# Kernel tuning notes

Hardware: AMD Instinct MI355X
Metric: run time of the kernel (lower is better)

## Reference

```python
import jax, jax.numpy as jnp
import numpy as np

B, N, D = 2, 2048, 1024
RANK, HEADS = 256, 16
HS = RANK // HEADS          # 16, low-rank head size for QK
DH = D // HEADS             # 64, value head size
SCALE = 1.0 / np.sqrt(HS)


def setup_inputs() -> dict:
    key = jax.random.key(0)
    k1, k2, k3 = jax.random.split(key, 3)
    x = jax.random.normal(k1, (B, N, D), dtype=jnp.float32)
    # causal additive mask, 0 on/below diag, -1e9 above
    mask = jnp.where(jnp.tril(jnp.ones((N, N), dtype=bool)), 0.0, -1e9).astype(jnp.float32)
    Wqk = jax.random.normal(k2, (2 * RANK, D), dtype=jnp.float32) * (1.0 / np.sqrt(D))
    Wv = jax.random.normal(k3, (D, D), dtype=jnp.float32) * (1.0 / np.sqrt(D))
    return {"x": x, "mask": mask, "Wqk": Wqk, "Wv": Wv}


def reference(x, mask, Wqk, Wv):
    b, n, d = x.shape
    qk = jnp.einsum('bnd,rd->bnr', x, Wqk)            # [b,n,2*rank]
    q, k = jnp.split(qk, 2, axis=-1)                  # [b,n,rank] each
    # L2 normalize over FULL rank dim (before head split), clamp norm >= 1e-6
    q = q / jnp.maximum(jnp.linalg.norm(q, axis=-1, keepdims=True), 1e-6)
    k = k / jnp.maximum(jnp.linalg.norm(k, axis=-1, keepdims=True), 1e-6)
    q = q.reshape(b, n, HEADS, HS).transpose(0, 2, 1, 3)   # [b,h,n,hs]
    k = k.reshape(b, n, HEADS, HS).transpose(0, 2, 1, 3)
    v = jnp.einsum('bnd,ed->bne', x, Wv).reshape(b, n, HEADS, DH).transpose(0, 2, 1, 3)  # [b,h,n,dh]
    att = jnp.einsum('bhqe,bhke->bhqk', q, k) * SCALE
    att = jnp.clip(att, -10000.0, 10000.0)
    att = att + mask[None, None, :, :]
    att = jax.nn.softmax(att, axis=-1)
    # NaN guard: zero NaNs then renormalize (no-op when no NaNs)
    att = jnp.where(jnp.isnan(att), 0.0, att)
    att = att / jnp.maximum(att.sum(axis=-1, keepdims=True), 1e-6)
    y = jnp.einsum('bhqk,bhkd->bhqd', att, v)              # [b,h,n,dh]
    return y.transpose(0, 2, 1, 3).reshape(b, n, d)
```

## Files before the change

kernel.cpp:

```cpp
#include <hip/hip_runtime.h>
#include <math.h>

#define BATCH 2
#define SEQ   2048
#define DIM   1024
#define RANK  256
#define HEADS 16
#define HS    16
#define DH    64
#define MROWS 4096

#define QSCALE 0.36067376f

typedef __attribute__((ext_vector_type(8)))  short    short8;
typedef __attribute__((ext_vector_type(4)))  float    f32x4;
typedef __attribute__((ext_vector_type(16))) float    f32x16;
typedef __attribute__((ext_vector_type(2)))  unsigned uint2v;

#define GPTR const __attribute__((address_space(1))) unsigned int*
#define LPTR __attribute__((address_space(3))) unsigned int*

__device__ __forceinline__ unsigned short f2bf(float f) {
    union { float f; unsigned u; } v; v.f = f;
    return (unsigned short)((v.u + 0x7FFFu + ((v.u >> 16) & 1u)) >> 16);
}
__device__ __forceinline__ float bf2f(unsigned short h) {
    union { unsigned u; float f; } v; v.u = ((unsigned)h) << 16;
    return v.f;
}

#define XQ   1048576
#define WQKQ 131072
#define WVQ  262144
__global__ __launch_bounds__(256) void conv3(const float* __restrict__ x,
                                             const float* __restrict__ wqk,
                                             const float* __restrict__ wv,
                                             unsigned short* __restrict__ xb,
                                             unsigned short* __restrict__ wcat)
{
    const int i = blockIdx.x * 256 + threadIdx.x;
    const float* src; unsigned short* dst; int j;
    if (i < XQ)              { src = x;   dst = xb;   j = i; }
    else if (i < XQ + WQKQ)  { src = wqk; dst = wcat; j = i - XQ; }
    else                     { src = wv;  dst = wcat + (size_t)4 * WQKQ; j = i - XQ - WQKQ; }
    float4 v = ((const float4*)src)[j];
    ushort4 o; o.x = f2bf(v.x); o.y = f2bf(v.y); o.z = f2bf(v.z); o.w = f2bf(v.w);
    ((ushort4*)dst)[j] = o;
}

__global__ __launch_bounds__(256, 3) void gemm_mfma(const unsigned short* __restrict__ A,
                                                    const unsigned short* __restrict__ W,
                                                    unsigned short* __restrict__ qkb,
                                                    unsigned short* __restrict__ vt)
{
    __shared__ __align__(16) unsigned short Alds[2][128 * 64];
    __shared__ __align__(16) unsigned short Blds[2][64 * 64];

    const int tid = threadIdx.x;
    const int w = tid >> 6, lane = tid & 63;
    const int lr = lane & 15, lg = lane >> 4;
    const int wm = w >> 1, wn = w & 1;

    const int Lf = blockIdx.x;
    const int wg = (Lf & 7) * 96 + (Lf >> 3);
    const int bm = (wg & 31) * 128;
    const int bn = (wg >> 5) * 64;

    const int rs = lane >> 3, cs = lane & 7;

    f32x4 acc[4][2] = {};

#define STAGEG(kt_, buf_) do {                                                        \
        const int k0_ = (kt_) * 64;                                                   \
        _Pragma("unroll")                                                             \
        for (int i = 0; i < 4; ++i) {                                                 \
            const int r = w * 32 + i * 8 + rs;                                        \
            __builtin_amdgcn_global_load_lds(                                         \
                (GPTR)&A[(size_t)(bm + r) * 1024 + k0_ + 8 * (cs ^ (r & 7))],         \
                (LPTR)&Alds[buf_][(w * 32 + i * 8) * 64], 16, 0, 0);                  \
        }                                                                             \
        _Pragma("unroll")                                                             \
        for (int i = 0; i < 2; ++i) {                                                 \
            const int r = w * 16 + i * 8 + rs;                                        \
            __builtin_amdgcn_global_load_lds(                                         \
                (GPTR)&W[(size_t)(bn + r) * 1024 + k0_ + 8 * (cs ^ (r & 7))],         \
                (LPTR)&Blds[buf_][(w * 16 + i * 8) * 64], 16, 0, 0);                  \
        }                                                                             \
    } while (0)

    STAGEG(0, 0);

    #pragma unroll 1
    for (int kt = 0; kt < 16; ++kt) {
        if (kt + 1 < 16) {
            STAGEG(kt + 1, (kt + 1) & 1);
            asm volatile("s_waitcnt vmcnt(6)" ::: "memory");
        } else {
            asm volatile("s_waitcnt vmcnt(0)" ::: "memory");
        }
        __builtin_amdgcn_sched_barrier(0);
        __builtin_amdgcn_s_barrier();

        const int buf = kt & 1;
        #pragma unroll
        for (int kk = 0; kk < 2; ++kk) {
            short8 af[4], bfr[2];
            #pragma unroll
            for (int mi = 0; mi < 4; ++mi) {
                const int row = wm * 64 + mi * 16 + lr;
                af[mi] = *(const short8*)&Alds[buf][row * 64 + 8 * ((kk * 4 + lg) ^ (row & 7))];
            }
            #pragma unroll
            for (int ni = 0; ni < 2; ++ni) {
                const int row = wn * 32 + ni * 16 + lr;
                bfr[ni] = *(const short8*)&Blds[buf][row * 64 + 8 * ((kk * 4 + lg) ^ (row & 7))];
            }
            #pragma unroll
            for (int mi = 0; mi < 4; ++mi)
                #pragma unroll
                for (int ni = 0; ni < 2; ++ni)
                    acc[mi][ni] = __builtin_amdgcn_mfma_f32_16x16x32_bf16(af[mi], bfr[ni], acc[mi][ni], 0, 0, 0);
        }
        __builtin_amdgcn_s_barrier();
    }
#undef STAGEG

    if (bn < 512) {
        #pragma unroll
        for (int mi = 0; mi < 4; ++mi) {
            const int rbase = bm + wm * 64 + mi * 16 + lg * 4;
            #pragma unroll
            for (int ni = 0; ni < 2; ++ni) {
                const int col = bn + wn * 32 + ni * 16 + lr;
                #pragma unroll
                for (int r = 0; r < 4; ++r)
                    qkb[(size_t)(rbase + r) * 512 + col] = f2bf(acc[mi][ni][r]);
            }
        }
    } else {
        const int nb = bn - 512;
        #pragma unroll
        for (int mi = 0; mi < 4; ++mi) {
            const int m = bm + wm * 64 + mi * 16 + lg * 4;
            const int bb = m >> 11, ms = m & 2047;
            #pragma unroll
            for (int ni = 0; ni < 2; ++ni) {
                const int d = nb + wn * 32 + ni * 16 + lr;
                ushort4 pk;
                pk.x = f2bf(acc[mi][ni][0]); pk.y = f2bf(acc[mi][ni][1]);
                pk.z = f2bf(acc[mi][ni][2]); pk.w = f2bf(acc[mi][ni][3]);
                *(ushort4*)&vt[((size_t)bb * DIM + d) * SEQ + ms] = pk;
            }
        }
    }
}

__global__ __launch_bounds__(256) void l2norm_split(const unsigned short* __restrict__ qkb,
                                                    unsigned short* __restrict__ qn,
                                                    unsigned short* __restrict__ kn)
{
    const int row = blockIdx.x;
    const int t = threadIdx.x;
    const unsigned short* p = qkb + (size_t)row * 512;
    float q = bf2f(p[t]);
    float k = bf2f(p[t + 256]);
    float sq = q * q, sk = k * k;
    #pragma unroll
    for (int off = 32; off > 0; off >>= 1) {
        sq += __shfl_down(sq, off);
        sk += __shfl_down(sk, off);
    }
    __shared__ float sh[8];
    const int wid = t >> 6;
    if ((t & 63) == 0) { sh[wid * 2] = sq; sh[wid * 2 + 1] = sk; }
    __syncthreads();
    sq = sh[0] + sh[2] + sh[4] + sh[6];
    sk = sh[1] + sh[3] + sh[5] + sh[7];
    const float rq = QSCALE / fmaxf(sqrtf(sq), 1e-6f);
    const float rk = 1.0f   / fmaxf(sqrtf(sk), 1e-6f);

    const int b = row >> 11, n = row & 2047;
    const int head = t >> 4, hs = t & 15;
    const size_t o = (((size_t)b * HEADS + head) * SEQ + n) * 16 + hs;
    qn[o] = f2bf(q * rq);
    kn[o] = f2bf(k * rk);
}


template<bool MASK>
__device__ __forceinline__ void segpv(const short8 ak0, const short8 ak1, const short8 bq,
                                      const unsigned short* Vs, int kb, int kh, int hi,
                                      int l31, int qg, f32x16 o[2], float& lp)
{
    const f32x16 z = {};
    short8 pa[4];

    const f32x16 s0 = __builtin_amdgcn_mfma_f32_32x32x16_bf16(ak0, bq, z, 0, 0, 0);
    {
        float p0[16];
        #pragma unroll
        for (int r = 0; r < 16; ++r) {
            float e = __builtin_exp2f(s0[r]);
            if (MASK) {
                const int kl = kb + (r & 3) + 8 * (r >> 2) + 4 * hi;
                e = (kl > qg) ? 0.0f : e;
            }
            p0[r] = e; lp += e;
        }
        #pragma unroll
        for (int g = 0; g < 2; ++g) {
            const int jj = 2 * g;
            unsigned a0, a1, b0, b1;
            asm("v_cvt_pk_bf16_f32 %0, %1, %2" : "=v"(a0) : "v"(p0[4*jj]),     "v"(p0[4*jj + 1]));
            asm("v_cvt_pk_bf16_f32 %0, %1, %2" : "=v"(b0) : "v"(p0[4*jj + 2]), "v"(p0[4*jj + 3]));
            asm("v_cvt_pk_bf16_f32 %0, %1, %2" : "=v"(a1) : "v"(p0[4*jj + 4]), "v"(p0[4*jj + 5]));
            asm("v_cvt_pk_bf16_f32 %0, %1, %2" : "=v"(b1) : "v"(p0[4*jj + 6]), "v"(p0[4*jj + 7]));
            const uint2v r0 = __builtin_amdgcn_permlane32_swap(a0, a1, false, false);
            const uint2v r1 = __builtin_amdgcn_permlane32_swap(b0, b1, false, false);
            union { short8 s; unsigned u[4]; } pu;
            pu.u[0] = r0[0]; pu.u[1] = r1[0]; pu.u[2] = r0[1]; pu.u[3] = r1[1];
            pa[g] = pu.s;
        }
    }
    const f32x16 s1 = __builtin_amdgcn_mfma_f32_32x32x16_bf16(ak1, bq, z, 0, 0, 0);
    {
        float p1[16];
        #pragma unroll
        for (int r = 0; r < 16; ++r) {
            float e = __builtin_exp2f(s1[r]);
            if (MASK) {
                const int kl = kb + 32 + (r & 3) + 8 * (r >> 2) + 4 * hi;
                e = (kl > qg) ? 0.0f : e;
            }
            p1[r] = e; lp += e;
        }
        #pragma unroll
        for (int g = 0; g < 2; ++g) {
            const int jj = 2 * g;
            unsigned a0, a1, b0, b1;
            asm("v_cvt_pk_bf16_f32 %0, %1, %2" : "=v"(a0) : "v"(p1[4*jj]),     "v"(p1[4*jj + 1]));
            asm("v_cvt_pk_bf16_f32 %0, %1, %2" : "=v"(b0) : "v"(p1[4*jj + 2]), "v"(p1[4*jj + 3]));
            asm("v_cvt_pk_bf16_f32 %0, %1, %2" : "=v"(a1) : "v"(p1[4*jj + 4]), "v"(p1[4*jj + 5]));
            asm("v_cvt_pk_bf16_f32 %0, %1, %2" : "=v"(b1) : "v"(p1[4*jj + 6]), "v"(p1[4*jj + 7]));
            const uint2v r0 = __builtin_amdgcn_permlane32_swap(a0, a1, false, false);
            const uint2v r1 = __builtin_amdgcn_permlane32_swap(b0, b1, false, false);
            union { short8 s; unsigned u[4]; } pu;
            pu.u[0] = r0[0]; pu.u[1] = r1[0]; pu.u[2] = r0[1]; pu.u[3] = r1[1];
            pa[2 + g] = pu.s;
        }
    }

    #pragma unroll
    for (int g = 0; g < 4; ++g)
        #pragma unroll
        for (int half = 0; half < 2; ++half) {
            const int row = half * 32 + l31;
            const int slot = (8 * kh + 2 * g + hi) ^ (row & 15);
            const short8 bv = *(const short8*)&Vs[row * 128 + 8 * slot];
            o[half] = __builtin_amdgcn_mfma_f32_32x32x16_bf16(pa[g], bv, o[half], 0, 0, 0);
        }
}

__global__ __launch_bounds__(512, 4) void attn_w8(const unsigned short* __restrict__ qn,
                                                  const unsigned short* __restrict__ kn,
                                                  const unsigned short* __restrict__ vt,
                                                  float* __restrict__ out)
{
    const int L = blockIdx.x;
    const int bh = L & 31;
    const int p  = L >> 5;
    const int h = bh & 15, b = bh >> 4;

    const int tid = threadIdx.x, w = tid >> 6, lane = tid & 63;
    const int seg = w >> 2, qh = (w >> 1) & 1, kh = w & 1;
    const int l31 = lane & 31, hi = lane >> 5;

    const int qt  = seg ? p : 31 - p;
    const int nts = (qt >> 1) + 1;
    const int nt0 = ((31 - p) >> 1) + 1;
    const int band = qt * 64 + qh * 32;
    const int qg = band + l31;

    __shared__ __align__(16) unsigned char smem[33792];

    const unsigned short* qbh = qn + (size_t)bh * SEQ * 16;
    const unsigned short* kbh = kn + (size_t)bh * SEQ * 16;

    const short8 bq = *(const short8*)&qbh[qg * 16 + 8 * hi];

    f32x16 o[2] = {};
    float lp = 0.0f;

    const unsigned short* kwin = kbh + (64 * kh + l31) * 16 + 8 * hi;
    short8 ak0 = *(const short8*)(kwin);
    short8 ak1 = *(const short8*)(kwin + 32 * 16);

    const int vsub = lane >> 4, vslot = lane & 15;

#define STAGEV(kt_, buf_) do {                                                                    \
        const int k0_ = (kt_) * 128;                                                              \
        _Pragma("unroll")                                                                         \
        for (int i = 0; i < 2; ++i) {                                                             \
            const int c = 2 * w + i;                                                              \
            const int dh = 4 * c + vsub;                                                          \
            const int so = 8 * (vslot ^ (dh & 15));                                               \
            __builtin_amdgcn_global_load_lds(                                                     \
                (GPTR)&vt[((size_t)b * DIM + h * DH + dh) * SEQ + k0_ + so],                      \
                (LPTR)(smem + (buf_) * 16384 + c * 1024), 16, 0, 0);                              \
        }                                                                                         \
    } while (0)

    STAGEV(0, 0);

    #pragma unroll 1
    for (int kt = 0; kt < nt0; ++kt) {
        short8 an0 = ak0, an1 = ak1;
        if (kt + 1 < nt0) {
            STAGEV(kt + 1, (kt + 1) & 1);
            an0 = *(const short8*)(kwin + (size_t)(kt + 1) * 128 * 16);
            an1 = *(const short8*)(kwin + (size_t)(kt + 1) * 128 * 16 + 32 * 16);
            asm volatile("s_waitcnt vmcnt(4)" ::: "memory");
        } else {
            asm volatile("s_waitcnt vmcnt(0)" ::: "memory");
        }
        __builtin_amdgcn_sched_barrier(0);
        __builtin_amdgcn_s_barrier();

        if (kt < nts) {
            const unsigned short* Vs = (const unsigned short*)(smem + (kt & 1) * 16384);
            const int kb = kt * 128 + 64 * kh;
            __builtin_amdgcn_s_setprio(1);
            if (kt < nts - 1) {
                segpv<false>(ak0, ak1, bq, Vs, kb, kh, hi, l31, qg, o, lp);
            } else if (kb <= band + 31) {
                if (kb + 63 <= band) segpv<false>(ak0, ak1, bq, Vs, kb, kh, hi, l31, qg, o, lp);
                else                 segpv<true >(ak0, ak1, bq, Vs, kb, kh, hi, l31, qg, o, lp);
            }
            __builtin_amdgcn_s_setprio(0);
        }

        ak0 = an0; ak1 = an1;
        __builtin_amdgcn_s_barrier();
    }
#undef STAGEV

    lp += __shfl_xor(lp, 32);

    __syncthreads();
    float* Os = (float*)(smem + seg * 16384);
    float* Ls = (float*)(smem + 32768 + seg * 512);

    if (kh == 1) {
        #pragma unroll
        for (int half = 0; half < 2; ++half)
            #pragma unroll
            for (int r = 0; r < 16; ++r) {
                const int q = (r & 3) + 8 * (r >> 2) + 4 * hi;
                Os[(qh * 32 + q) * 64 + half * 32 + l31] = o[half][r];
            }
        Ls[qh * 64 + lane] = lp;
    }
    __syncthreads();
    if (kh == 0) {
        const float lt = lp + Ls[qh * 64 + lane];
        const float inv = 1.0f / fmaxf(lt, 1e-6f);
        #pragma unroll
        for (int r = 0; r < 16; ++r) {
            const int q = (r & 3) + 8 * (r >> 2) + 4 * hi;
            const float iv = __shfl(inv, q);
            #pragma unroll
            for (int half = 0; half < 2; ++half) {
                const float v = (o[half][r] + Os[(qh * 32 + q) * 64 + half * 32 + l31]) * iv;
                __builtin_nontemporal_store(v,
                    &out[((size_t)b * SEQ + band + q) * DIM + h * DH + half * 32 + l31]);
            }
        }
    }
}

extern "C" void kernel_launch(void* const* d_in, const int* in_sizes, int n_in,
                              void* d_out, int out_size, void* d_ws, size_t ws_size,
                              hipStream_t stream)
{
    const float* x   = (const float*)d_in[0];
    const float* Wqk = (const float*)d_in[2];
    const float* Wv  = (const float*)d_in[3];
    float* out = (float*)d_out;

    unsigned short* xb   = (unsigned short*)d_ws;
    unsigned short* qkb  = xb  + (size_t)MROWS * DIM;
    unsigned short* vt   = qkb + (size_t)MROWS * 512;
    unsigned short* wcat = vt  + (size_t)BATCH * DIM * SEQ;
    unsigned short* qn = xb;
    unsigned short* kn = xb + (size_t)32 * SEQ * 16;

    conv3<<<5632, 256, 0, stream>>>(x, Wqk, Wv, xb, wcat);
    gemm_mfma<<<768, 256, 0, stream>>>(xb, wcat, qkb, vt);
    l2norm_split<<<MROWS, 256, 0, stream>>>(qkb, qn, kn);
    attn_w8<<<512, 512, 0, stream>>>(qn, kn, vt, out);
}
```

Before: 68.74 us.

## Pre-swizzle V into MFMA fragment layout and drop LDS staging in attention

The GEMM epilogue now writes V in a per-head tiled layout that matches the MFMA B-operand fragments, so the attention kernel can load V directly from global memory into registers. The attention kernel is restructured so each wave owns a whole 32-query band over all key tiles, with band assignments balanced across the causal triangle, and runs 256 threads per block. This removes the LDS double buffering, the barriers and the cross-wave reduction of partial outputs. In exchange every wave reads V from global/L2 itself with no sharing, and there is no explicit prefetch overlap for the V loads.

```diff
diff --git a/kernel.cpp b/kernel.cpp
--- a/kernel.cpp
+++ b/kernel.cpp
@@ -51,7 +51,7 @@
 __global__ __launch_bounds__(256, 3) void gemm_mfma(const unsigned short* __restrict__ A,
                                                     const unsigned short* __restrict__ W,
                                                     unsigned short* __restrict__ qkb,
-                                                    unsigned short* __restrict__ vt)
+                                                    unsigned short* __restrict__ vt2)
 {
     __shared__ __align__(16) unsigned short Alds[2][128 * 64];
     __shared__ __align__(16) unsigned short Blds[2][64 * 64];
@@ -142,14 +142,19 @@
         #pragma unroll
         for (int mi = 0; mi < 4; ++mi) {
             const int m = bm + wm * 64 + mi * 16 + lg * 4;
-            const int bb = m >> 11, ms = m & 2047;
+            const int bb = m >> 11, k = m & 2047;
             #pragma unroll
             for (int ni = 0; ni < 2; ++ni) {
                 const int d = nb + wn * 32 + ni * 16 + lr;
+                const int h = d >> 6, dh = d & 63;
                 ushort4 pk;
                 pk.x = f2bf(acc[mi][ni][0]); pk.y = f2bf(acc[mi][ni][1]);
                 pk.z = f2bf(acc[mi][ni][2]); pk.w = f2bf(acc[mi][ni][3]);
-                *(ushort4*)&vt[((size_t)bb * DIM + d) * SEQ + ms] = pk;
+                const size_t off = (size_t)(bb * HEADS + h) * (SEQ * 64)
+                                 + (k >> 6) * 4096 + ((k >> 4) & 3) * 1024
+                                 + (dh >> 5) * 512 + (dh & 31) * 16
+                                 + ((k >> 3) & 1) * 8 + (k & 7);
+                *(ushort4*)&vt2[off] = pk;
             }
         }
     }
@@ -188,9 +193,8 @@
 
 
 template<bool MASK>
-__device__ __forceinline__ void segpv(const short8 ak0, const short8 ak1, const short8 bq,
-                                      const unsigned short* Vs, int kb, int kh, int hi,
-                                      int l31, int qg, f32x16 o[2], float& lp)
+__device__ __forceinline__ void tile_nb(const short8 ak0, const short8 ak1, const short8 bq,
+                                        const short8 vb[4][2], int hi, f32x16 o[2], float& lp)
 {
     const f32x16 z = {};
     short8 pa[4];
@@ -202,11 +206,13 @@
         for (int r = 0; r < 16; ++r) {
             float e = __builtin_exp2f(s0[r]);
             if (MASK) {
-                const int kl = kb + (r & 3) + 8 * (r >> 2) + 4 * hi;
-                e = (kl > qg) ? 0.0f : e;
-            }
-            p0[r] = e; lp += e;
-        }
+                const int kl = (r & 3) + 8 * (r >> 2) + 4 * hi;
+                e = (kl > 0) ? 0.0f : e;
+            }
+            p0[r] = e;
+        }
+        #pragma unroll
+        for (int r = 0; r < 16; ++r) lp += p0[r];
         #pragma unroll
         for (int g = 0; g < 2; ++g) {
             const int jj = 2 * g;
@@ -227,11 +233,7 @@
         float p1[16];
         #pragma unroll
         for (int r = 0; r < 16; ++r) {
-            float e = __builtin_exp2f(s1[r]);
-            if (MASK) {
-                const int kl = kb + 32 + (r & 3) + 8 * (r >> 2) + 4 * hi;
-                e = (kl > qg) ? 0.0f : e;
-            }
+            const float e = __builtin_exp2f(s1[r]);
             p1[r] = e; lp += e;
         }
         #pragma unroll
@@ -253,127 +255,118 @@
     #pragma unroll
     for (int g = 0; g < 4; ++g)
         #pragma unroll
-        for (int half = 0; half < 2; ++half) {
-            const int row = half * 32 + l31;
-            const int slot = (8 * kh + 2 * g + hi) ^ (row & 15);
-            const short8 bv = *(const short8*)&Vs[row * 128 + 8 * slot];
-            o[half] = __builtin_amdgcn_mfma_f32_32x32x16_bf16(pa[g], bv, o[half], 0, 0, 0);
-        }
-}
-
-__global__ __launch_bounds__(512, 4) void attn_w8(const unsigned short* __restrict__ qn,
+        for (int half = 0; half < 2; ++half)
+            o[half] = __builtin_amdgcn_mfma_f32_32x32x16_bf16(pa[g], vb[g][half], o[half], 0, 0, 0);
+}
+
+__device__ __forceinline__ void tile_nb_mask(const short8 ak0, const short8 ak1, const short8 bq,
+                                             const short8 vb[4][2], int kb, int hi, int qg,
+                                             f32x16 o[2], float& lp)
+{
+    const f32x16 z = {};
+    short8 pa[4];
+    const f32x16 s0 = __builtin_amdgcn_mfma_f32_32x32x16_bf16(ak0, bq, z, 0, 0, 0);
+    const f32x16 s1 = __builtin_amdgcn_mfma_f32_32x32x16_bf16(ak1, bq, z, 0, 0, 0);
+    float p0[16], p1[16];
+    #pragma unroll
+    for (int r = 0; r < 16; ++r) {
+        const int kl = kb + (r & 3) + 8 * (r >> 2) + 4 * hi;
+        float e0 = __builtin_exp2f(s0[r]);
+        float e1 = __builtin_exp2f(s1[r]);
+        e0 = (kl > qg) ? 0.0f : e0;
+        e1 = (kl + 32 > qg) ? 0.0f : e1;
+        p0[r] = e0; p1[r] = e1;
+        lp += e0 + e1;
+    }
+    #pragma unroll
+    for (int g = 0; g < 4; ++g) {
+        const float* pc = (g < 2) ? p0 : p1;
+        const int jj = 2 * (g & 1);
+        unsigned a0, a1, b0, b1;
+        asm("v_cvt_pk_bf16_f32 %0, %1, %2" : "=v"(a0) : "v"(pc[4*jj]),     "v"(pc[4*jj + 1]));
+        asm("v_cvt_pk_bf16_f32 %0, %1, %2" : "=v"(b0) : "v"(pc[4*jj + 2]), "v"(pc[4*jj + 3]));
+        asm("v_cvt_pk_bf16_f32 %0, %1, %2" : "=v"(a1) : "v"(pc[4*jj + 4]), "v"(pc[4*jj + 5]));
+        asm("v_cvt_pk_bf16_f32 %0, %1, %2" : "=v"(b1) : "v"(pc[4*jj + 6]), "v"(pc[4*jj + 7]));
+        const uint2v r0 = __builtin_amdgcn_permlane32_swap(a0, a1, false, false);
+        const uint2v r1 = __builtin_amdgcn_permlane32_swap(b0, b1, false, false);
+        union { short8 s; unsigned u[4]; } pu;
+        pu.u[0] = r0[0]; pu.u[1] = r1[0]; pu.u[2] = r0[1]; pu.u[3] = r1[1];
+        pa[g] = pu.s;
+    }
+    #pragma unroll
+    for (int g = 0; g < 4; ++g)
+        #pragma unroll
+        for (int half = 0; half < 2; ++half)
+            o[half] = __builtin_amdgcn_mfma_f32_32x32x16_bf16(pa[g], vb[g][half], o[half], 0, 0, 0);
+}
+
+__global__ __launch_bounds__(256, 2) void attn_nb(const unsigned short* __restrict__ qn,
                                                   const unsigned short* __restrict__ kn,
-                                                  const unsigned short* __restrict__ vt,
+                                                  const unsigned short* __restrict__ vt2,
                                                   float* __restrict__ out)
 {
     const int L = blockIdx.x;
     const int bh = L & 31;
-    const int p  = L >> 5;
+    const int j  = L >> 5;
     const int h = bh & 15, b = bh >> 4;
 
     const int tid = threadIdx.x, w = tid >> 6, lane = tid & 63;
-    const int seg = w >> 2, qh = (w >> 1) & 1, kh = w & 1;
     const int l31 = lane & 31, hi = lane >> 5;
 
-    const int qt  = seg ? p : 31 - p;
-    const int nts = (qt >> 1) + 1;
-    const int nt0 = ((31 - p) >> 1) + 1;
-    const int band = qt * 64 + qh * 32;
-    const int qg = band + l31;
-
-    __shared__ __align__(16) unsigned char smem[33792];
+    const int band = (w == 0) ? j : (w == 1) ? 63 - j : (w == 2) ? 31 - j : 32 + j;
+    const int nts = (band >> 1) + 1;
+    const int qg = band * 32 + l31;
 
     const unsigned short* qbh = qn + (size_t)bh * SEQ * 16;
     const unsigned short* kbh = kn + (size_t)bh * SEQ * 16;
-
-    const short8 bq = *(const short8*)&qbh[qg * 16 + 8 * hi];
+    const unsigned short* vbh = vt2 + (size_t)bh * (SEQ * 64);
+
+    const short8 bq = *(const short8*)&qbh[(size_t)qg * 16 + 8 * hi];
 
     f32x16 o[2] = {};
     float lp = 0.0f;
 
-    const unsigned short* kwin = kbh + (64 * kh + l31) * 16 + 8 * hi;
+    const unsigned short* kwin = kbh + l31 * 16 + 8 * hi;
+    const unsigned short* vwin = vbh + l31 * 16 + hi * 8;
+
     short8 ak0 = *(const short8*)(kwin);
     short8 ak1 = *(const short8*)(kwin + 32 * 16);
 
-    const int vsub = lane >> 4, vslot = lane & 15;
-
-#define STAGEV(kt_, buf_) do {                                                                    \
-        const int k0_ = (kt_) * 128;                                                              \
-        _Pragma("unroll")                                                                         \
-        for (int i = 0; i < 2; ++i) {                                                             \
-            const int c = 2 * w + i;                                                              \
-            const int dh = 4 * c + vsub;                                                          \
-            const int so = 8 * (vslot ^ (dh & 15));                                               \
-            __builtin_amdgcn_global_load_lds(                                                     \
-                (GPTR)&vt[((size_t)b * DIM + h * DH + dh) * SEQ + k0_ + so],                      \
-                (LPTR)(smem + (buf_) * 16384 + c * 1024), 16, 0, 0);                              \
-        }                                                                                         \
-    } while (0)
-
-    STAGEV(0, 0);
-
     #pragma unroll 1
-    for (int kt = 0; kt < nt0; ++kt) {
+    for (int t = 0; t < nts; ++t) {
+        short8 vb[4][2];
+        #pragma unroll
+        for (int g = 0; g < 4; ++g)
+            #pragma unroll
+            for (int half = 0; half < 2; ++half)
+                vb[g][half] = *(const short8*)(vwin + (size_t)t * 4096 + g * 1024 + half * 512);
+
         short8 an0 = ak0, an1 = ak1;
-        if (kt + 1 < nt0) {
-            STAGEV(kt + 1, (kt + 1) & 1);
-            an0 = *(const short8*)(kwin + (size_t)(kt + 1) * 128 * 16);
-            an1 = *(const short8*)(kwin + (size_t)(kt + 1) * 128 * 16 + 32 * 16);
-            asm volatile("s_waitcnt vmcnt(4)" ::: "memory");
-        } else {
-            asm volatile("s_waitcnt vmcnt(0)" ::: "memory");
-        }
-        __builtin_amdgcn_sched_barrier(0);
-        __builtin_amdgcn_s_barrier();
-
-        if (kt < nts) {
-            const unsigned short* Vs = (const unsigned short*)(smem + (kt & 1) * 16384);
-            const int kb = kt * 128 + 64 * kh;
-            __builtin_amdgcn_s_setprio(1);
-            if (kt < nts - 1) {
-                segpv<false>(ak0, ak1, bq, Vs, kb, kh, hi, l31, qg, o, lp);
-            } else if (kb <= band + 31) {
-                if (kb + 63 <= band) segpv<false>(ak0, ak1, bq, Vs, kb, kh, hi, l31, qg, o, lp);
-                else                 segpv<true >(ak0, ak1, bq, Vs, kb, kh, hi, l31, qg, o, lp);
-            }
-            __builtin_amdgcn_s_setprio(0);
-        }
+        if (t + 1 < nts) {
+            an0 = *(const short8*)(kwin + (size_t)(t + 1) * 1024);
+            an1 = *(const short8*)(kwin + (size_t)(t + 1) * 1024 + 32 * 16);
+        }
+
+        if (t < nts - 1)
+            tile_nb<false>(ak0, ak1, bq, vb, hi, o, lp);
+        else
+            tile_nb_mask(ak0, ak1, bq, vb, t * 64, hi, qg, o, lp);
 
         ak0 = an0; ak1 = an1;
-        __builtin_amdgcn_s_barrier();
-    }
-#undef STAGEV
+    }
 
     lp += __shfl_xor(lp, 32);
-
-    __syncthreads();
-    float* Os = (float*)(smem + seg * 16384);
-    float* Ls = (float*)(smem + 32768 + seg * 512);
-
-    if (kh == 1) {
-        #pragma unroll
-        for (int half = 0; half < 2; ++half)
-            #pragma unroll
-            for (int r = 0; r < 16; ++r) {
-                const int q = (r & 3) + 8 * (r >> 2) + 4 * hi;
-                Os[(qh * 32 + q) * 64 + half * 32 + l31] = o[half][r];
-            }
-        Ls[qh * 64 + lane] = lp;
-    }
-    __syncthreads();
-    if (kh == 0) {
-        const float lt = lp + Ls[qh * 64 + lane];
-        const float inv = 1.0f / fmaxf(lt, 1e-6f);
-        #pragma unroll
-        for (int r = 0; r < 16; ++r) {
-            const int q = (r & 3) + 8 * (r >> 2) + 4 * hi;
-            const float iv = __shfl(inv, q);
-            #pragma unroll
-            for (int half = 0; half < 2; ++half) {
-                const float v = (o[half][r] + Os[(qh * 32 + q) * 64 + half * 32 + l31]) * iv;
-                __builtin_nontemporal_store(v,
-                    &out[((size_t)b * SEQ + band + q) * DIM + h * DH + half * 32 + l31]);
-            }
+    const float inv = 1.0f / fmaxf(lp, 1e-6f);
+
+    #pragma unroll
+    for (int r = 0; r < 16; ++r) {
+        const int q = (r & 3) + 8 * (r >> 2) + 4 * hi;
+        const float iv = __shfl(inv, q);
+        #pragma unroll
+        for (int half = 0; half < 2; ++half) {
+            const float v = o[half][r] * iv;
+            __builtin_nontemporal_store(v,
+                &out[((size_t)b * SEQ + band * 32 + q) * DIM + h * DH + half * 32 + l31]);
         }
     }
 }
@@ -389,13 +382,13 @@
 
     unsigned short* xb   = (unsigned short*)d_ws;
     unsigned short* qkb  = xb  + (size_t)MROWS * DIM;
-    unsigned short* vt   = qkb + (size_t)MROWS * 512;
-    unsigned short* wcat = vt  + (size_t)BATCH * DIM * SEQ;
+    unsigned short* vt2  = qkb + (size_t)MROWS * 512;
+    unsigned short* wcat = vt2 + (size_t)BATCH * DIM * SEQ;
     unsigned short* qn = xb;
     unsigned short* kn = xb + (size_t)32 * SEQ * 16;
 
     conv3<<<5632, 256, 0, stream>>>(x, Wqk, Wv, xb, wcat);
-    gemm_mfma<<<768, 256, 0, stream>>>(xb, wcat, qkb, vt);
+    gemm_mfma<<<768, 256, 0, stream>>>(xb, wcat, qkb, vt2);
     l2norm_split<<<MROWS, 256, 0, stream>>>(qkb, qn, kn);
-    attn_w8<<<512, 512, 0, stream>>>(qn, kn, vt, out);
-}
+    attn_nb<<<512, 256, 0, stream>>>(qn, kn, vt2, out);
+}
```

Result: slower. 72.79 us (+5.9%).

## Fuse fp32-to-bf16 conversion into GEMM staging, drop separate convert kernel

Applied to the files above, without the earlier changes.

Removes the conv3 kernel and has the GEMM load fp32 x and weights directly into registers, convert them with packed bf16 conversion instructions, and write them into swizzled LDS. This saves one launch and the bf16 round trip through global memory. In exchange, the GEMM now reads twice as many bytes per tile and each of the 768 blocks re-converts its tiles. The async global-to-LDS path is also replaced by register-staged prefetch, which adds register pressure and uses a single barrier per iteration.

```diff
diff --git a/kernel.cpp b/kernel.cpp
--- a/kernel.cpp
+++ b/kernel.cpp
@@ -29,29 +29,11 @@
     return v.f;
 }
 
-#define XQ   1048576
-#define WQKQ 131072
-#define WVQ  262144
-__global__ __launch_bounds__(256) void conv3(const float* __restrict__ x,
-                                             const float* __restrict__ wqk,
-                                             const float* __restrict__ wv,
-                                             unsigned short* __restrict__ xb,
-                                             unsigned short* __restrict__ wcat)
-{
-    const int i = blockIdx.x * 256 + threadIdx.x;
-    const float* src; unsigned short* dst; int j;
-    if (i < XQ)              { src = x;   dst = xb;   j = i; }
-    else if (i < XQ + WQKQ)  { src = wqk; dst = wcat; j = i - XQ; }
-    else                     { src = wv;  dst = wcat + (size_t)4 * WQKQ; j = i - XQ - WQKQ; }
-    float4 v = ((const float4*)src)[j];
-    ushort4 o; o.x = f2bf(v.x); o.y = f2bf(v.y); o.z = f2bf(v.z); o.w = f2bf(v.w);
-    ((ushort4*)dst)[j] = o;
-}
-
-__global__ __launch_bounds__(256, 3) void gemm_mfma(const unsigned short* __restrict__ A,
-                                                    const unsigned short* __restrict__ W,
-                                                    unsigned short* __restrict__ qkb,
-                                                    unsigned short* __restrict__ vt)
+__global__ __launch_bounds__(256, 3) void gemm_fused(const float* __restrict__ A,
+                                                     const float* __restrict__ Wqk,
+                                                     const float* __restrict__ Wv,
+                                                     unsigned short* __restrict__ qkb,
+                                                     unsigned short* __restrict__ vt)
 {
     __shared__ __align__(16) unsigned short Alds[2][128 * 64];
     __shared__ __align__(16) unsigned short Blds[2][64 * 64];
@@ -66,39 +48,49 @@
     const int bm = (wg & 31) * 128;
     const int bn = (wg >> 5) * 64;
 
-    const int rs = lane >> 3, cs = lane & 7;
+    const float* Wsrc = (bn < 512) ? (Wqk + (size_t)bn * 1024)
+                                   : (Wv + (size_t)(bn - 512) * 1024);
+
+    const int rsub = tid >> 4;
+    const int kq   = tid & 15;
+
+    float4 avreg[8], bvreg[4];
+
+#define LOADF(kt_) do { const int k0_ = (kt_) * 64;                                               \
+        _Pragma("unroll") for (int jj = 0; jj < 8; ++jj)                                          \
+            avreg[jj] = *(const float4*)&A[(size_t)(bm + jj * 16 + rsub) * 1024 + k0_ + 4 * kq];  \
+        _Pragma("unroll") for (int jj = 0; jj < 4; ++jj)                                          \
+            bvreg[jj] = *(const float4*)&Wsrc[(size_t)(jj * 16 + rsub) * 1024 + k0_ + 4 * kq];    \
+    } while (0)
+
+#define CVTWR(buf_) do {                                                                          \
+        _Pragma("unroll") for (int jj = 0; jj < 8; ++jj) {                                        \
+            const int r = jj * 16 + rsub;                                                         \
+            unsigned u0, u1;                                                                      \
+            asm("v_cvt_pk_bf16_f32 %0, %1, %2" : "=v"(u0) : "v"(avreg[jj].x), "v"(avreg[jj].y));  \
+            asm("v_cvt_pk_bf16_f32 %0, %1, %2" : "=v"(u1) : "v"(avreg[jj].z), "v"(avreg[jj].w));  \
+            uint2 pkv; pkv.x = u0; pkv.y = u1;                                                    \
+            *(uint2*)((char*)&Alds[buf_][0] + r * 128 + 16 * ((kq >> 1) ^ (r & 7)) + 8 * (kq & 1)) = pkv; \
+        }                                                                                         \
+        _Pragma("unroll") for (int jj = 0; jj < 4; ++jj) {                                        \
+            const int r = jj * 16 + rsub;                                                         \
+            unsigned u0, u1;                                                                      \
+            asm("v_cvt_pk_bf16_f32 %0, %1, %2" : "=v"(u0) : "v"(bvreg[jj].x), "v"(bvreg[jj].y));  \
+            asm("v_cvt_pk_bf16_f32 %0, %1, %2" : "=v"(u1) : "v"(bvreg[jj].z), "v"(bvreg[jj].w));  \
+            uint2 pkv; pkv.x = u0; pkv.y = u1;                                                    \
+            *(uint2*)((char*)&Blds[buf_][0] + r * 128 + 16 * ((kq >> 1) ^ (r & 7)) + 8 * (kq & 1)) = pkv; \
+        }                                                                                         \
+    } while (0)
 
     f32x4 acc[4][2] = {};
 
-#define STAGEG(kt_, buf_) do {                                                        \
-        const int k0_ = (kt_) * 64;                                                   \
-        _Pragma("unroll")                                                             \
-        for (int i = 0; i < 4; ++i) {                                                 \
-            const int r = w * 32 + i * 8 + rs;                                        \
-            __builtin_amdgcn_global_load_lds(                                         \
-                (GPTR)&A[(size_t)(bm + r) * 1024 + k0_ + 8 * (cs ^ (r & 7))],         \
-                (LPTR)&Alds[buf_][(w * 32 + i * 8) * 64], 16, 0, 0);                  \
-        }                                                                             \
-        _Pragma("unroll")                                                             \
-        for (int i = 0; i < 2; ++i) {                                                 \
-            const int r = w * 16 + i * 8 + rs;                                        \
-            __builtin_amdgcn_global_load_lds(                                         \
-                (GPTR)&W[(size_t)(bn + r) * 1024 + k0_ + 8 * (cs ^ (r & 7))],         \
-                (LPTR)&Blds[buf_][(w * 16 + i * 8) * 64], 16, 0, 0);                  \
-        }                                                                             \
-    } while (0)
-
-    STAGEG(0, 0);
+    LOADF(0);
+    CVTWR(0);
 
     #pragma unroll 1
     for (int kt = 0; kt < 16; ++kt) {
-        if (kt + 1 < 16) {
-            STAGEG(kt + 1, (kt + 1) & 1);
-            asm volatile("s_waitcnt vmcnt(6)" ::: "memory");
-        } else {
-            asm volatile("s_waitcnt vmcnt(0)" ::: "memory");
-        }
-        __builtin_amdgcn_sched_barrier(0);
+        if (kt + 1 < 16) LOADF(kt + 1);
+        asm volatile("s_waitcnt lgkmcnt(0)" ::: "memory");
         __builtin_amdgcn_s_barrier();
 
         const int buf = kt & 1;
@@ -121,9 +113,11 @@
                 for (int ni = 0; ni < 2; ++ni)
                     acc[mi][ni] = __builtin_amdgcn_mfma_f32_16x16x32_bf16(af[mi], bfr[ni], acc[mi][ni], 0, 0, 0);
         }
-        __builtin_amdgcn_s_barrier();
-    }
-#undef STAGEG
+
+        if (kt + 1 < 16) CVTWR((kt + 1) & 1);
+    }
+#undef LOADF
+#undef CVTWR
 
     if (bn < 512) {
         #pragma unroll
@@ -185,7 +179,6 @@
     qn[o] = f2bf(q * rq);
     kn[o] = f2bf(k * rk);
 }
-
 
 template<bool MASK>
 __device__ __forceinline__ void segpv(const short8 ak0, const short8 ak1, const short8 bq,
@@ -387,15 +380,12 @@
     const float* Wv  = (const float*)d_in[3];
     float* out = (float*)d_out;
 
-    unsigned short* xb   = (unsigned short*)d_ws;
-    unsigned short* qkb  = xb  + (size_t)MROWS * DIM;
-    unsigned short* vt   = qkb + (size_t)MROWS * 512;
-    unsigned short* wcat = vt  + (size_t)BATCH * DIM * SEQ;
-    unsigned short* qn = xb;
-    unsigned short* kn = xb + (size_t)32 * SEQ * 16;
-
-    conv3<<<5632, 256, 0, stream>>>(x, Wqk, Wv, xb, wcat);
-    gemm_mfma<<<768, 256, 0, stream>>>(xb, wcat, qkb, vt);
+    unsigned short* qkb = (unsigned short*)d_ws;
+    unsigned short* vt  = qkb + (size_t)MROWS * 512;
+    unsigned short* qn  = vt  + (size_t)BATCH * DIM * SEQ;
+    unsigned short* kn  = qn  + (size_t)32 * SEQ * 16;
+
+    gemm_fused<<<768, 256, 0, stream>>>(x, Wqk, Wv, qkb, vt);
     l2norm_split<<<MROWS, 256, 0, stream>>>(qkb, qn, kn);
     attn_w8<<<512, 512, 0, stream>>>(qn, kn, vt, out);
 }
```

Measured after the change: 87.02 us. +26.6%, slower.
